# Kernel optimization log

Hardware: AMD Instinct MI355X
Metric: run time of the kernel (lower is better)

Reference implementation:

```python
import jax, jax.numpy as jnp
import numpy as np

H = 4096      # hidden_size
NH = 32       # num heads
HD = H // NH  # head_dim = 128
I = 11008     # intermediate_size
T = 2048      # num tokens (single prompt sequence)
G = 128       # AWQ group size
EPS = 1e-6
ROPE_BASE = 10000.0


def _make_qlinear(key, k_in, n_out):
    k1, k2, k3 = jax.random.split(key, 3)
    qw = jax.random.randint(k1, (k_in, n_out), 0, 16, dtype=jnp.int32)
    qz = jax.random.randint(k2, (k_in // G, n_out), 0, 16, dtype=jnp.int32)
    scales = jax.random.uniform(k3, (k_in // G, n_out), dtype=jnp.float32) * 0.01 + 1e-3
    return qw, scales, qz


def setup_inputs() -> dict:
    key = jax.random.key(0)
    ks = jax.random.split(key, 8)
    inp = {
        "positions": jnp.arange(T, dtype=jnp.int64),
        "hidden_states": jax.random.normal(ks[0], (T, H), dtype=jnp.float32),
        "input_ln_w": jnp.ones((H,), dtype=jnp.float32),
        "post_ln_w": jnp.ones((H,), dtype=jnp.float32),
    }
    inp["qkv_qw"], inp["qkv_scales"], inp["qkv_qz"] = _make_qlinear(ks[1], H, 3 * H)
    inp["o_qw"], inp["o_scales"], inp["o_qz"] = _make_qlinear(ks[2], H, H)
    inp["gu_qw"], inp["gu_scales"], inp["gu_qz"] = _make_qlinear(ks[3], H, 2 * I)
    inp["down_qw"], inp["down_scales"], inp["down_qz"] = _make_qlinear(ks[4], I, H)
    return inp


def rms_norm(x, w):
    var = jnp.mean(x * x, axis=-1, keepdims=True)
    return x * jax.lax.rsqrt(var + EPS) * w


def awq_linear(x, qw, scales, qz):
    # dequant: (q - z) * scale, group-wise along K; then dense GEMM
    w = (qw.astype(scales.dtype) - jnp.repeat(qz.astype(scales.dtype), G, axis=0)) \
        * jnp.repeat(scales, G, axis=0)
    return x @ w


def apply_rope(x, positions):
    # x: [T, NH, HD], neox-style half rotation, rotary_dim = HD
    inv_freq = 1.0 / (ROPE_BASE ** (jnp.arange(0, HD, 2, dtype=jnp.float32) / HD))
    ang = positions.astype(jnp.float32)[:, None] * inv_freq  # [T, HD/2]
    cos = jnp.cos(ang)[:, None, :]
    sin = jnp.sin(ang)[:, None, :]
    x1, x2 = x[..., : HD // 2], x[..., HD // 2:]
    return jnp.concatenate([x1 * cos - x2 * sin, x2 * cos + x1 * sin], axis=-1)


def reference(positions, hidden_states, input_ln_w, post_ln_w,
              qkv_qw, qkv_scales, qkv_qz, o_qw, o_scales, o_qz,
              gu_qw, gu_scales, gu_qz, down_qw, down_scales, down_qz):
    residual = hidden_states
    x = rms_norm(hidden_states, input_ln_w)

    # attention
    qkv = awq_linear(x, qkv_qw, qkv_scales, qkv_qz)  # [T, 3H]
    q, k, v = jnp.split(qkv, 3, axis=-1)
    q = apply_rope(q.reshape(T, NH, HD), positions)
    k = apply_rope(k.reshape(T, NH, HD), positions)
    v = v.reshape(T, NH, HD)
    scale = HD ** -0.5
    scores = jnp.einsum('qhd,khd->hqk', q, k) * scale  # [NH, T, T]
    causal = jnp.tril(jnp.ones((T, T), dtype=bool))
    scores = jnp.where(causal[None], scores, jnp.finfo(scores.dtype).min)
    probs = jax.nn.softmax(scores, axis=-1)
    attn = jnp.einsum('hqk,khd->qhd', probs, v).reshape(T, H)
    attn_out = awq_linear(attn, o_qw, o_scales, o_qz)

    hidden = residual + attn_out
    residual = hidden
    x = rms_norm(hidden, post_ln_w)

    # MLP: gate_up -> silu(gate) * up -> down
    gate_up = awq_linear(x, gu_qw, gu_scales, gu_qz)  # [T, 2I]
    gate, up = jnp.split(gate_up, 2, axis=-1)
    x = jax.nn.silu(gate) * up
    x = awq_linear(x, down_qw, down_scales, down_qz)
    return residual + x
```

## Files before the change

kernel.cpp:

```cpp
#include <hip/hip_runtime.h>
#include <stdint.h>

#define T_SEQ 2048
#define HID 4096
#define NHEADS 32
#define I_FF 11008
#define QKV_N 12288
#define GU_N 22016

typedef unsigned short u16;
typedef unsigned int u32;
typedef __attribute__((ext_vector_type(4))) float f32x4;
typedef __attribute__((ext_vector_type(8))) __bf16 bf16x8;
typedef __attribute__((ext_vector_type(4))) u32 u32x4;
typedef __attribute__((ext_vector_type(2))) u32 u32x2;

__device__ __forceinline__ u16 f2bf(float f) {
  union { float f; u32 u; } v; v.f = f;
  u32 u = v.u;
  return (u16)((u + 0x7fffu + ((u >> 16) & 1u)) >> 16);
}
__device__ __forceinline__ float bf2f(u16 h) {
  union { u32 u; float f; } v; v.u = ((u32)h) << 16;
  return v.f;
}
__device__ __forceinline__ void split2(float x, u16& hi, u16& lo) {
  hi = f2bf(x);
  lo = f2bf(x - bf2f(hi));
}
__device__ __forceinline__ void split8(const float* v, u32x4& H, u32x4& L) {
#pragma unroll
  for (int j = 0; j < 4; j++) {
    u16 h0, l0, h1, l1;
    split2(v[2 * j], h0, l0);
    split2(v[2 * j + 1], h1, l1);
    H[j] = (u32)h0 | ((u32)h1 << 16);
    L[j] = (u32)l0 | ((u32)l1 << 16);
  }
}
__device__ __forceinline__ void dq8(u32 rbp, int zq, u32x4& w) {
#pragma unroll
  for (int j = 0; j < 4; j++) {
    int q0 = (int)((rbp >> (8 * j)) & 15u) - zq;
    int q1 = (int)((rbp >> (8 * j + 4)) & 15u) - zq;
    u32 b0 = __builtin_bit_cast(u32, (float)q0);
    u32 b1 = __builtin_bit_cast(u32, (float)q1);
    w[j] = (b0 >> 16) | (b1 & 0xffff0000u);
  }
}

__global__ __launch_bounds__(256) void pack_qw_kernel(
    const int* __restrict__ qw, u32* __restrict__ pw, int N) {
  int n = blockIdx.x * 256 + threadIdx.x;
  int oct = blockIdx.y;
  const int* src = qw + (size_t)oct * 8 * N + n;
  u32 v = 0;
#pragma unroll
  for (int j = 0; j < 8; j++)
    v |= ((u32)src[(size_t)j * N] & 15u) << (4 * j);
  pw[(size_t)oct * N + n] = v;
}

__global__ __launch_bounds__(256) void rmsnorm_kernel(
    const float* __restrict__ in, const float* __restrict__ w,
    u16* __restrict__ outh) {
  int row = blockIdx.x;
  const float* x = in + (size_t)row * HID;
  float4 vals[4];
  float ss = 0.f;
#pragma unroll
  for (int k = 0; k < 4; k++) {
    vals[k] = ((const float4*)x)[threadIdx.x + k * 256];
    ss += vals[k].x * vals[k].x + vals[k].y * vals[k].y +
          vals[k].z * vals[k].z + vals[k].w * vals[k].w;
  }
#pragma unroll
  for (int o = 1; o < 64; o <<= 1) ss += __shfl_xor(ss, o);
  __shared__ float red[4];
  if ((threadIdx.x & 63) == 0) red[threadIdx.x >> 6] = ss;
  __syncthreads();
  ss = red[0] + red[1] + red[2] + red[3];
  float rs = rsqrtf(ss * (1.f / HID) + 1e-6f);
#pragma unroll
  for (int k = 0; k < 4; k++) {
    int c4 = threadIdx.x + k * 256;
    float4 wv = ((const float4*)w)[c4];
    float o[4] = {vals[k].x * rs * wv.x, vals[k].y * rs * wv.y,
                  vals[k].z * rs * wv.z, vals[k].w * rs * wv.w};
    u32x2 H;
    H[0] = (u32)f2bf(o[0]) | ((u32)f2bf(o[1]) << 16);
    H[1] = (u32)f2bf(o[2]) | ((u32)f2bf(o[3]) << 16);
    *(u32x2*)(outh + (size_t)row * HID + c4 * 4) = H;
  }
}

template <bool RESID, bool OUTBF16>
__global__ __launch_bounds__(512) void awq_gemm256_kernel(
    const u16* __restrict__ Ahg,
    const u32* __restrict__ pw, const float* __restrict__ scales,
    const int* __restrict__ qz, const float* __restrict__ resid,
    void* __restrict__ outp, int N, int K, int nstrips) {
  __shared__ u16 AhL[2][128][40];
  __shared__ u16 BqL[2][256][40];
  int tid = threadIdx.x;
  int lane = tid & 63;
  int wid = tid >> 6;
  int g16 = lane >> 4, l16 = lane & 15;
  int p = blockIdx.x;
  int xcd = p & 7;
  int idx = p >> 3;
  int s = idx >> 1;
  int mi = ((idx & 1) << 3) + xcd;
  if (s >= nstrips) return;
  int m0 = mi * 128;
  int n0 = s * 256;
  int wr = wid >> 2, wc = wid & 3;

  f32x4 acc[4][4] = {};
  float svold[4];

  int a_row = tid >> 2, a_kc = (tid & 3) * 8;
  const u16* aph = Ahg + (size_t)(m0 + a_row) * K + a_kc;
  int b_n = tid & 255;
  int b_oct = (tid >> 8) * 2;
  int b_kb = b_oct * 8;
  const u32* pwp = pw + (size_t)b_oct * N + n0 + b_n;
  const float* scp = scales + n0;
  const int* qzp = qz + n0 + b_n;

  int nsteps = K >> 5;

  u32x4 rah;
  u32 rb0, rb1;

  auto load_step = [&](int ks) {
    int k0 = ks << 5;
    rah = *(const u32x4*)(aph + k0);
    const u32* q = pwp + (size_t)(ks << 2) * N;
    rb0 = q[0];
    rb1 = q[N];
  };
  auto write_step = [&](int buf, int zq) {
    *(u32x4*)&AhL[buf][a_row][a_kc] = rah;
    u32x4 w0, w1;
    dq8(rb0, zq, w0);
    dq8(rb1, zq, w1);
    *(u32x4*)&BqL[buf][b_n][b_kb] = w0;
    *(u32x4*)&BqL[buf][b_n][b_kb + 8] = w1;
  };

  int zq = qzp[0];
  load_step(0);
  write_step(0, zq);
#pragma unroll
  for (int n = 0; n < 4; n++)
    svold[n] = scp[wc * 64 + n * 16 + l16];
  __syncthreads();

  int cur = 0;
  for (int ks = 0; ks < nsteps; ks++) {
    int nxt = ks + 1;
    if (nxt < nsteps) {
      if ((nxt & 3) == 0) zq = qzp[(size_t)(nxt >> 2) * N];
      load_step(nxt);
    }
    if (ks != 0 && (ks & 3) == 0) {
      int g = ks >> 2;
#pragma unroll
      for (int n = 0; n < 4; n++) {
        float svnew = scp[(size_t)g * N + wc * 64 + n * 16 + l16];
        float r = svold[n] * __builtin_amdgcn_rcpf(svnew);
        svold[n] = svnew;
#pragma unroll
        for (int m = 0; m < 4; m++)
#pragma unroll
          for (int i = 0; i < 4; i++) acc[m][n][i] *= r;
      }
    }
    bf16x8 bq[4];
#pragma unroll
    for (int n = 0; n < 4; n++)
      bq[n] = __builtin_bit_cast(bf16x8,
          *(const u32x4*)&BqL[cur][wc * 64 + n * 16 + l16][g16 * 8]);
#pragma unroll
    for (int m = 0; m < 4; m++) {
      bf16x8 ah = __builtin_bit_cast(bf16x8,
          *(const u32x4*)&AhL[cur][wr * 64 + m * 16 + l16][g16 * 8]);
#pragma unroll
      for (int n = 0; n < 4; n++)
        acc[m][n] = __builtin_amdgcn_mfma_f32_16x16x32_bf16(ah, bq[n], acc[m][n], 0, 0, 0);
    }
    if (nxt < nsteps) write_step(cur ^ 1, zq);
    __syncthreads();
    cur ^= 1;
  }
#pragma unroll
  for (int n = 0; n < 4; n++)
#pragma unroll
    for (int m = 0; m < 4; m++)
#pragma unroll
      for (int i = 0; i < 4; i++) acc[m][n][i] *= svold[n];
#pragma unroll
  for (int m = 0; m < 4; m++) {
#pragma unroll
    for (int n = 0; n < 4; n++) {
#pragma unroll
      for (int r = 0; r < 4; r++) {
        int row = m0 + wr * 64 + m * 16 + g16 * 4 + r;
        int col = n0 + wc * 64 + n * 16 + l16;
        float v = acc[m][n][r];
        if (RESID) v += resid[(size_t)row * N + col];
        if (OUTBF16)
          ((u16*)outp)[(size_t)row * N + col] = f2bf(v);
        else
          ((float*)outp)[(size_t)row * N + col] = v;
      }
    }
  }
}

__global__ __launch_bounds__(256) void rope_kernel(float* __restrict__ qkv) {
  int t = blockIdx.x;
  __shared__ float cs[64], sn[64];
  if (threadIdx.x < 64) {
    int i = threadIdx.x;
    float freq = exp2f(-(float)i * (13.287712379549449f / 64.f));
    float ang = (float)t * freq;
    cs[i] = cosf(ang);
    sn[i] = sinf(ang);
  }
  __syncthreads();
#pragma unroll
  for (int it = 0; it < 16; it++) {
    int idx = threadIdx.x + it * 256;
    int part = idx >> 11;
    int rem = idx & 2047;
    int hh = rem >> 6, i = rem & 63;
    float* base = qkv + (size_t)t * QKV_N + (size_t)part * HID + hh * 128;
    float x1 = base[i], x2 = base[64 + i];
    float c = cs[i], s = sn[i];
    base[i] = x1 * c - x2 * s;
    base[64 + i] = x2 * c + x1 * s;
  }
}

__global__ __launch_bounds__(256) void transpose_v_kernel(
    const float* __restrict__ qkv, u16* __restrict__ vt) {
  __shared__ u16 tile[64][65];
  int tb = blockIdx.x;
  int cb = blockIdx.y;
  int tid = threadIdx.x;
  int r = tid >> 2, c16 = (tid & 3) * 16;
  const float* src = qkv + (size_t)(tb * 64 + r) * QKV_N + 2 * HID + cb * 64 + c16;
  float v[16];
  *(float4*)&v[0] = *(const float4*)(src);
  *(float4*)&v[4] = *(const float4*)(src + 4);
  *(float4*)&v[8] = *(const float4*)(src + 8);
  *(float4*)&v[12] = *(const float4*)(src + 12);
#pragma unroll
  for (int i = 0; i < 16; i++) tile[r][c16 + i] = f2bf(v[i]);
  __syncthreads();
  int ocol = tid >> 2, tchunk = (tid & 3) * 16;
  u16 vbuf[16];
#pragma unroll
  for (int i = 0; i < 16; i++) vbuf[i] = tile[tchunk + i][ocol];
  u16* dst = vt + (size_t)(cb * 64 + ocol) * T_SEQ + tb * 64 + tchunk;
  *(u32x4*)dst = *(u32x4*)&vbuf[0];
  *(u32x4*)(dst + 8) = *(u32x4*)&vbuf[8];
}

__global__ __launch_bounds__(256) void attn_kernel(
    const float* __restrict__ qkv, const u16* __restrict__ vt,
    u16* __restrict__ outh) {
  constexpr float SCALE = 0.08838834764831845f;
  __shared__ u16 Kh[32][136], Kl[32][136];
  __shared__ u16 Vt_lds[128][40];
  __shared__ u16 P_lds[4][16][40];
  int tid = threadIdx.x;
  int wid = tid >> 6, lane = tid & 63;
  int g16 = lane >> 4, l16 = lane & 15;
  int h = blockIdx.x & 31;
  int qt = blockIdx.x >> 5;
  int qb = qt * 64;

  bf16x8 qh[4], ql[4];
  {
    const float* qsrc = qkv + (size_t)(qb + wid * 16 + l16) * QKV_N + h * 128;
#pragma unroll
    for (int ds = 0; ds < 4; ds++) {
      float v[8];
      *(float4*)&v[0] = *(const float4*)(qsrc + ds * 32 + g16 * 8);
      *(float4*)&v[4] = *(const float4*)(qsrc + ds * 32 + g16 * 8 + 4);
      u32x4 H, L;
      split8(v, H, L);
      qh[ds] = __builtin_bit_cast(bf16x8, H);
      ql[ds] = __builtin_bit_cast(bf16x8, L);
    }
  }
  f32x4 oacc[8] = {};
  float mrun[4] = {-1e30f, -1e30f, -1e30f, -1e30f};
  float lrun[4] = {0.f, 0.f, 0.f, 0.f};

  int st_k = tid >> 3, st_d = (tid & 7) * 16;
  int sv_d = tid >> 1, sv_k = (tid & 1) * 16;

  int ktiles = (qb + 64) >> 5;
  for (int kt = 0; kt < ktiles; kt++) {
    __syncthreads();
    {
      const float* src = qkv + (size_t)(kt * 32 + st_k) * QKV_N + HID + h * 128 + st_d;
      float v[16];
      *(float4*)&v[0] = *(const float4*)(src);
      *(float4*)&v[4] = *(const float4*)(src + 4);
      *(float4*)&v[8] = *(const float4*)(src + 8);
      *(float4*)&v[12] = *(const float4*)(src + 12);
      u32x4 H, L;
      split8(&v[0], H, L);
      *(u32x4*)&Kh[st_k][st_d] = H;
      *(u32x4*)&Kl[st_k][st_d] = L;
      split8(&v[8], H, L);
      *(u32x4*)&Kh[st_k][st_d + 8] = H;
      *(u32x4*)&Kl[st_k][st_d + 8] = L;
    }
    {
      const u16* src = vt + (size_t)(h * 128 + sv_d) * T_SEQ + kt * 32 + sv_k;
      *(u32x4*)&Vt_lds[sv_d][sv_k] = *(const u32x4*)src;
      *(u32x4*)&Vt_lds[sv_d][sv_k + 8] = *(const u32x4*)(src + 8);
    }
    __syncthreads();
    f32x4 sacc[2] = {};
#pragma unroll
    for (int kb = 0; kb < 2; kb++)
#pragma unroll
      for (int ds = 0; ds < 4; ds++) {
        bf16x8 kfh = __builtin_bit_cast(bf16x8,
            *(const u32x4*)&Kh[kb * 16 + l16][ds * 32 + g16 * 8]);
        bf16x8 kfl = __builtin_bit_cast(bf16x8,
            *(const u32x4*)&Kl[kb * 16 + l16][ds * 32 + g16 * 8]);
        sacc[kb] = __builtin_amdgcn_mfma_f32_16x16x32_bf16(qh[ds], kfh, sacc[kb], 0, 0, 0);
        sacc[kb] = __builtin_amdgcn_mfma_f32_16x16x32_bf16(ql[ds], kfh, sacc[kb], 0, 0, 0);
        sacc[kb] = __builtin_amdgcn_mfma_f32_16x16x32_bf16(qh[ds], kfl, sacc[kb], 0, 0, 0);
      }
    float p0v[4], p1v[4];
#pragma unroll
    for (int r = 0; r < 4; r++) {
      int qrow = qb + wid * 16 + g16 * 4 + r;
      bool msk0 = (kt * 32 + l16) > qrow;
      bool msk1 = (kt * 32 + 16 + l16) > qrow;
      float s0 = msk0 ? -1e30f : sacc[0][r] * SCALE;
      float s1 = msk1 ? -1e30f : sacc[1][r] * SCALE;
      float tm = fmaxf(s0, s1);
      tm = fmaxf(tm, __shfl_xor(tm, 1));
      tm = fmaxf(tm, __shfl_xor(tm, 2));
      tm = fmaxf(tm, __shfl_xor(tm, 4));
      tm = fmaxf(tm, __shfl_xor(tm, 8));
      float mnew = fmaxf(mrun[r], tm);
      float fac = __expf(mrun[r] - mnew);
      float p0 = msk0 ? 0.f : __expf(s0 - mnew);
      float p1 = msk1 ? 0.f : __expf(s1 - mnew);
      float ts = p0 + p1;
      ts += __shfl_xor(ts, 1);
      ts += __shfl_xor(ts, 2);
      ts += __shfl_xor(ts, 4);
      ts += __shfl_xor(ts, 8);
      lrun[r] = lrun[r] * fac + ts;
      mrun[r] = mnew;
      p0v[r] = p0; p1v[r] = p1;
#pragma unroll
      for (int db = 0; db < 8; db++) oacc[db][r] *= fac;
    }
#pragma unroll
    for (int r = 0; r < 4; r++) {
      P_lds[wid][g16 * 4 + r][l16] = f2bf(p0v[r]);
      P_lds[wid][g16 * 4 + r][16 + l16] = f2bf(p1v[r]);
    }
    __syncthreads();
    bf16x8 pa = __builtin_bit_cast(bf16x8, *(const u32x4*)&P_lds[wid][l16][g16 * 8]);
#pragma unroll
    for (int db = 0; db < 8; db++) {
      bf16x8 vb = __builtin_bit_cast(bf16x8,
          *(const u32x4*)&Vt_lds[db * 16 + l16][g16 * 8]);
      oacc[db] = __builtin_amdgcn_mfma_f32_16x16x32_bf16(pa, vb, oacc[db], 0, 0, 0);
    }
  }
#pragma unroll
  for (int r = 0; r < 4; r++) {
    int qrow = qb + wid * 16 + g16 * 4 + r;
    float inv = 1.f / lrun[r];
#pragma unroll
    for (int db = 0; db < 8; db++)
      outh[(size_t)qrow * HID + h * 128 + db * 16 + l16] =
          f2bf(oacc[db][r] * inv);
  }
}

__global__ __launch_bounds__(256) void silu_mul_kernel(
    const u16* __restrict__ gu, u16* __restrict__ acth) {
  size_t e = ((size_t)blockIdx.x * 256 + threadIdx.x) * 8;
  size_t row = e / I_FF;
  int col = (int)(e % I_FF);
  const u16* gp = gu + row * GU_N + col;
  u32x4 gv = *(const u32x4*)gp;
  u32x4 uv = *(const u32x4*)(gp + I_FF);
  u32x4 H;
#pragma unroll
  for (int j = 0; j < 4; j++) {
    float g0 = bf2f((u16)(gv[j] & 0xffff)), g1 = bf2f((u16)(gv[j] >> 16));
    float u0 = bf2f((u16)(uv[j] & 0xffff)), u1 = bf2f((u16)(uv[j] >> 16));
    float o0 = g0 / (1.f + __expf(-g0)) * u0;
    float o1 = g1 / (1.f + __expf(-g1)) * u1;
    H[j] = (u32)f2bf(o0) | ((u32)f2bf(o1) << 16);
  }
  *(u32x4*)(acth + row * I_FF + col) = H;
}

extern "C" void kernel_launch(void* const* d_in, const int* in_sizes, int n_in,
                              void* d_out, int out_size, void* d_ws, size_t ws_size,
                              hipStream_t stream) {
  const float* hs    = (const float*)d_in[1];
  const float* ln1   = (const float*)d_in[2];
  const float* ln2   = (const float*)d_in[3];
  const int* qkv_qw  = (const int*)d_in[4];
  const float* qkv_s = (const float*)d_in[5];
  const int* qkv_z   = (const int*)d_in[6];
  const int* o_qw    = (const int*)d_in[7];
  const float* o_s   = (const float*)d_in[8];
  const int* o_z     = (const int*)d_in[9];
  const int* gu_qw   = (const int*)d_in[10];
  const float* gu_s  = (const float*)d_in[11];
  const int* gu_z    = (const int*)d_in[12];
  const int* dn_qw   = (const int*)d_in[13];
  const float* dn_s  = (const float*)d_in[14];
  const int* dn_z    = (const int*)d_in[15];

  char* ws = (char*)d_ws;
  u16*   xnh    = (u16*)(ws);
  float* qkv    = (float*)(ws + (size_t)33554432);
  u16*   vt     = (u16*)(ws + (size_t)134217728);
  float* hidden = (float*)(ws + (size_t)150994944);
  u16*   gup    = (u16*)(ws + (size_t)184549376);
  u16*   attnh  = xnh;
  u16*   acth   = (u16*)qkv;
  u32* pk_gup = (u32*)gup;
  u32* pk_qkv = (u32*)((char*)qkv + (size_t)50331648);

  auto grid256 = [](int N) { return 16 * (N / 256); };

  rmsnorm_kernel<<<T_SEQ, 256, 0, stream>>>(hs, ln1, xnh);
  pack_qw_kernel<<<dim3(QKV_N / 256, HID / 8), 256, 0, stream>>>(qkv_qw, pk_gup, QKV_N);
  awq_gemm256_kernel<false, false><<<grid256(QKV_N), 512, 0, stream>>>(
      xnh, pk_gup, qkv_s, qkv_z, nullptr, qkv, QKV_N, HID, QKV_N / 256);
  rope_kernel<<<T_SEQ, 256, 0, stream>>>(qkv);
  transpose_v_kernel<<<dim3(T_SEQ / 64, HID / 64), 256, 0, stream>>>(qkv, vt);
  attn_kernel<<<NHEADS * (T_SEQ / 64), 256, 0, stream>>>(qkv, vt, attnh);
  pack_qw_kernel<<<dim3(HID / 256, HID / 8), 256, 0, stream>>>(o_qw, pk_gup, HID);
  awq_gemm256_kernel<true, false><<<grid256(HID), 512, 0, stream>>>(
      attnh, pk_gup, o_s, o_z, hs, hidden, HID, HID, HID / 256);
  rmsnorm_kernel<<<T_SEQ, 256, 0, stream>>>(hidden, ln2, xnh);
  pack_qw_kernel<<<dim3(GU_N / 256, HID / 8), 256, 0, stream>>>(gu_qw, pk_qkv, GU_N);
  awq_gemm256_kernel<false, true><<<grid256(GU_N), 512, 0, stream>>>(
      xnh, pk_qkv, gu_s, gu_z, nullptr, gup, GU_N, HID, GU_N / 256);
  silu_mul_kernel<<<(T_SEQ * (size_t)I_FF / 8 / 256), 256, 0, stream>>>(gup, acth);
  pack_qw_kernel<<<dim3(HID / 256, I_FF / 8), 256, 0, stream>>>(dn_qw, pk_gup, HID);
  awq_gemm256_kernel<true, false><<<grid256(HID), 512, 0, stream>>>(
      acth, pk_gup, dn_s, dn_z, hidden, (float*)d_out, HID, I_FF, HID / 256);
}
```

Baseline: 1.634 ms.

## Dequantize B fragments in registers directly from global, dropping B LDS staging

The AWQ GEMM no longer stages dequantized weights in shared memory. Each lane loads the packed int4 words for its own MFMA B fragment straight from global memory and dequantizes them in registers, using the packed bf16 convert instruction. This removes the B-tile LDS writes and reads and halves LDS use. The cost is that every wave row group (wr) redundantly loads and dequantizes the same weights, and global loads become narrower and more scattered.

```diff
diff --git a/kernel.cpp b/kernel.cpp
--- a/kernel.cpp
+++ b/kernel.cpp
@@ -38,15 +38,18 @@
     L[j] = (u32)l0 | ((u32)l1 << 16);
   }
 }
-__device__ __forceinline__ void dq8(u32 rbp, int zq, u32x4& w) {
+__device__ __forceinline__ bf16x8 dqfrag(u32 rbp, int zq) {
+  u32x4 w;
 #pragma unroll
   for (int j = 0; j < 4; j++) {
     int q0 = (int)((rbp >> (8 * j)) & 15u) - zq;
     int q1 = (int)((rbp >> (8 * j + 4)) & 15u) - zq;
-    u32 b0 = __builtin_bit_cast(u32, (float)q0);
-    u32 b1 = __builtin_bit_cast(u32, (float)q1);
-    w[j] = (b0 >> 16) | (b1 & 0xffff0000u);
-  }
+    float f0 = (float)q0, f1 = (float)q1;
+    u32 r;
+    asm("v_cvt_pk_bf16_f32 %0, %1, %2" : "=v"(r) : "v"(f0), "v"(f1));
+    w[j] = r;
+  }
+  return __builtin_bit_cast(bf16x8, w);
 }
 
 __global__ __launch_bounds__(256) void pack_qw_kernel(
@@ -95,13 +98,12 @@
 }
 
 template <bool RESID, bool OUTBF16>
-__global__ __launch_bounds__(512) void awq_gemm256_kernel(
+__global__ __launch_bounds__(512) void awq_gemm256r_kernel(
     const u16* __restrict__ Ahg,
     const u32* __restrict__ pw, const float* __restrict__ scales,
     const int* __restrict__ qz, const float* __restrict__ resid,
     void* __restrict__ outp, int N, int K, int nstrips) {
   __shared__ u16 AhL[2][128][40];
-  __shared__ u16 BqL[2][256][40];
   int tid = threadIdx.x;
   int lane = tid & 63;
   int wid = tid >> 6;
@@ -118,57 +120,46 @@
 
   f32x4 acc[4][4] = {};
   float svold[4];
+  int zqv[4];
 
   int a_row = tid >> 2, a_kc = (tid & 3) * 8;
   const u16* aph = Ahg + (size_t)(m0 + a_row) * K + a_kc;
-  int b_n = tid & 255;
-  int b_oct = (tid >> 8) * 2;
-  int b_kb = b_oct * 8;
-  const u32* pwp = pw + (size_t)b_oct * N + n0 + b_n;
-  const float* scp = scales + n0;
-  const int* qzp = qz + n0 + b_n;
+  int colb = n0 + wc * 64 + l16;
+  const u32* pwl = pw + (size_t)g16 * N + colb;
+  const int* qzl = qz + colb;
+  const float* scl = scales + n0;
 
   int nsteps = K >> 5;
 
-  u32x4 rah;
-  u32 rb0, rb1;
-
-  auto load_step = [&](int ks) {
-    int k0 = ks << 5;
-    rah = *(const u32x4*)(aph + k0);
-    const u32* q = pwp + (size_t)(ks << 2) * N;
-    rb0 = q[0];
-    rb1 = q[N];
-  };
-  auto write_step = [&](int buf, int zq) {
-    *(u32x4*)&AhL[buf][a_row][a_kc] = rah;
-    u32x4 w0, w1;
-    dq8(rb0, zq, w0);
-    dq8(rb1, zq, w1);
-    *(u32x4*)&BqL[buf][b_n][b_kb] = w0;
-    *(u32x4*)&BqL[buf][b_n][b_kb + 8] = w1;
-  };
-
-  int zq = qzp[0];
-  load_step(0);
-  write_step(0, zq);
-#pragma unroll
-  for (int n = 0; n < 4; n++)
-    svold[n] = scp[wc * 64 + n * 16 + l16];
+  u32x4 rah, rahn;
+  u32 rbv[4], rbn[4];
+
+  rah = *(const u32x4*)(aph);
+#pragma unroll
+  for (int n = 0; n < 4; n++) rbv[n] = pwl[n * 16];
+  *(u32x4*)&AhL[0][a_row][a_kc] = rah;
+#pragma unroll
+  for (int n = 0; n < 4; n++) {
+    zqv[n] = qzl[n * 16];
+    svold[n] = scl[wc * 64 + n * 16 + l16];
+  }
   __syncthreads();
 
   int cur = 0;
   for (int ks = 0; ks < nsteps; ks++) {
     int nxt = ks + 1;
     if (nxt < nsteps) {
-      if ((nxt & 3) == 0) zq = qzp[(size_t)(nxt >> 2) * N];
-      load_step(nxt);
+      rahn = *(const u32x4*)(aph + (nxt << 5));
+      const u32* q = pwl + (size_t)(nxt << 2) * N;
+#pragma unroll
+      for (int n = 0; n < 4; n++) rbn[n] = q[n * 16];
     }
     if (ks != 0 && (ks & 3) == 0) {
       int g = ks >> 2;
 #pragma unroll
       for (int n = 0; n < 4; n++) {
-        float svnew = scp[(size_t)g * N + wc * 64 + n * 16 + l16];
+        zqv[n] = qzl[(size_t)g * N + n * 16];
+        float svnew = scl[(size_t)g * N + wc * 64 + n * 16 + l16];
         float r = svold[n] * __builtin_amdgcn_rcpf(svnew);
         svold[n] = svnew;
 #pragma unroll
@@ -179,9 +170,7 @@
     }
     bf16x8 bq[4];
 #pragma unroll
-    for (int n = 0; n < 4; n++)
-      bq[n] = __builtin_bit_cast(bf16x8,
-          *(const u32x4*)&BqL[cur][wc * 64 + n * 16 + l16][g16 * 8]);
+    for (int n = 0; n < 4; n++) bq[n] = dqfrag(rbv[n], zqv[n]);
 #pragma unroll
     for (int m = 0; m < 4; m++) {
       bf16x8 ah = __builtin_bit_cast(bf16x8,
@@ -190,7 +179,11 @@
       for (int n = 0; n < 4; n++)
         acc[m][n] = __builtin_amdgcn_mfma_f32_16x16x32_bf16(ah, bq[n], acc[m][n], 0, 0, 0);
     }
-    if (nxt < nsteps) write_step(cur ^ 1, zq);
+    if (nxt < nsteps) {
+      *(u32x4*)&AhL[cur ^ 1][a_row][a_kc] = rahn;
+#pragma unroll
+      for (int n = 0; n < 4; n++) rbv[n] = rbn[n];
+    }
     __syncthreads();
     cur ^= 1;
   }
@@ -448,20 +441,20 @@
 
   rmsnorm_kernel<<<T_SEQ, 256, 0, stream>>>(hs, ln1, xnh);
   pack_qw_kernel<<<dim3(QKV_N / 256, HID / 8), 256, 0, stream>>>(qkv_qw, pk_gup, QKV_N);
-  awq_gemm256_kernel<false, false><<<grid256(QKV_N), 512, 0, stream>>>(
+  awq_gemm256r_kernel<false, false><<<grid256(QKV_N), 512, 0, stream>>>(
       xnh, pk_gup, qkv_s, qkv_z, nullptr, qkv, QKV_N, HID, QKV_N / 256);
   rope_kernel<<<T_SEQ, 256, 0, stream>>>(qkv);
   transpose_v_kernel<<<dim3(T_SEQ / 64, HID / 64), 256, 0, stream>>>(qkv, vt);
   attn_kernel<<<NHEADS * (T_SEQ / 64), 256, 0, stream>>>(qkv, vt, attnh);
   pack_qw_kernel<<<dim3(HID / 256, HID / 8), 256, 0, stream>>>(o_qw, pk_gup, HID);
-  awq_gemm256_kernel<true, false><<<grid256(HID), 512, 0, stream>>>(
+  awq_gemm256r_kernel<true, false><<<grid256(HID), 512, 0, stream>>>(
       attnh, pk_gup, o_s, o_z, hs, hidden, HID, HID, HID / 256);
   rmsnorm_kernel<<<T_SEQ, 256, 0, stream>>>(hidden, ln2, xnh);
   pack_qw_kernel<<<dim3(GU_N / 256, HID / 8), 256, 0, stream>>>(gu_qw, pk_qkv, GU_N);
-  awq_gemm256_kernel<false, true><<<grid256(GU_N), 512, 0, stream>>>(
+  awq_gemm256r_kernel<false, true><<<grid256(GU_N), 512, 0, stream>>>(
       xnh, pk_qkv, gu_s, gu_z, nullptr, gup, GU_N, HID, GU_N / 256);
   silu_mul_kernel<<<(T_SEQ * (size_t)I_FF / 8 / 256), 256, 0, stream>>>(gup, acth);
   pack_qw_kernel<<<dim3(HID / 256, I_FF / 8), 256, 0, stream>>>(dn_qw, pk_gup, HID);
-  awq_gemm256_kernel<true, false><<<grid256(HID), 512, 0, stream>>>(
+  awq_gemm256r_kernel<true, false><<<grid256(HID), 512, 0, stream>>>(
       acth, pk_gup, dn_s, dn_z, hidden, (float*)d_out, HID, I_FF, HID / 256);
 }
```

After: 1.900 ms. +16.3%, slower.
